# Kernel optimization log

Measured on AMD Instinct MI355X. Metric: run time of the kernel, lower is better.

Reference implementation:

```python
import jax, jax.numpy as jnp
import numpy as np

D_MODEL = 1024
NHEAD = 16
D_K = D_MODEL // NHEAD


def setup_inputs() -> dict:
    key = jax.random.key(0)
    ks = jax.random.split(key, 8)
    B, S = 2, 2048
    scale = 1.0 / np.sqrt(D_MODEL)
    return {
        "Q": jax.random.normal(ks[0], (B, S, D_MODEL), dtype=jnp.float32),
        "K": jax.random.normal(ks[1], (B, S, D_MODEL), dtype=jnp.float32),
        "V": jax.random.normal(ks[2], (B, S, D_MODEL), dtype=jnp.float32),
        "WQ": jax.random.normal(ks[3], (D_MODEL, D_MODEL), dtype=jnp.float32) * scale,
        "WK": jax.random.normal(ks[4], (D_MODEL, D_MODEL), dtype=jnp.float32) * scale,
        "WV": jax.random.normal(ks[5], (D_MODEL, D_MODEL), dtype=jnp.float32) * scale,
        "Wfc": jax.random.normal(ks[6], (D_MODEL, D_MODEL), dtype=jnp.float32) * scale,
        "bfc": jax.random.normal(ks[7], (D_MODEL,), dtype=jnp.float32) * 0.01,
    }


def reference(Q, K, V, WQ, WK, WV, Wfc, bfc):
    B, Sq, _ = Q.shape
    Skv = K.shape[1]
    # Linear projections (torch Linear: x @ W^T), split into heads: [B, H, S, d_k]
    q = (Q @ WQ.T).reshape(B, Sq, NHEAD, D_K).transpose(0, 2, 1, 3)
    k = (K @ WK.T).reshape(B, Skv, NHEAD, D_K).transpose(0, 2, 1, 3)
    v = (V @ WV.T).reshape(B, Skv, NHEAD, D_K).transpose(0, 2, 1, 3)
    # Scaled dot-product scores: [B, H, Sq, Skv]
    scores = jnp.einsum("bhqd,bhkd->bhqk", q, k) / jnp.sqrt(jnp.float32(D_K))
    # Causal mask (strict upper triangle -> -inf)
    causal = jnp.tril(jnp.ones((Sq, Skv), dtype=bool))
    scores = jnp.where(causal, scores, -jnp.inf)
    attn = jax.nn.softmax(scores, axis=-1)
    y = jnp.einsum("bhqk,bhkd->bhqd", attn, v)
    y = y.transpose(0, 2, 1, 3).reshape(B, Sq, D_MODEL)
    return y @ Wfc.T + bfc
```

## Files before the change

### kernel.cpp

```cpp
#include <hip/hip_runtime.h>

typedef __attribute__((ext_vector_type(8))) short bf16x8;
typedef __attribute__((ext_vector_type(4))) float f32x4;
typedef __attribute__((ext_vector_type(16))) float f32x16;

__device__ __forceinline__ ushort f2bf(float f) {
    union { float f; unsigned u; } x; x.f = f;
    unsigned r = x.u + 0x7fffu + ((x.u >> 16) & 1u);
    return (ushort)(r >> 16);
}

__device__ __forceinline__ void async16(const void* g, void* l) {
    __builtin_amdgcn_global_load_lds(
        (const __attribute__((address_space(1))) void*)g,
        (__attribute__((address_space(3))) void*)l, 16, 0, 0);
}

__device__ __forceinline__ f32x4 mfma16(bf16x8 a, bf16x8 b, f32x4 c) {
    return __builtin_amdgcn_mfma_f32_16x16x32_bf16(a, b, c, 0, 0, 0);
}
__device__ __forceinline__ f32x16 mfma32(bf16x8 a, bf16x8 b, f32x16 c) {
    return __builtin_amdgcn_mfma_f32_32x32x16_bf16(a, b, c, 0, 0, 0);
}

__device__ __forceinline__ f32x4 zero4() { f32x4 z = {0.f, 0.f, 0.f, 0.f}; return z; }

__global__ void cvt7_kernel(
    const float* __restrict__ s0, const float* __restrict__ s1, const float* __restrict__ s2,
    const float* __restrict__ s3, const float* __restrict__ s4, const float* __restrict__ s5,
    const float* __restrict__ s6,
    ushort* __restrict__ d0, ushort* __restrict__ d1, ushort* __restrict__ d2,
    ushort* __restrict__ d3, ushort* __restrict__ d4, ushort* __restrict__ d5,
    ushort* __restrict__ d6)
{
    int y = blockIdx.y;
    const float* s; ushort* d; int n4;
    if      (y == 0) { s = s0; d = d0; n4 = 1048576; }
    else if (y == 1) { s = s1; d = d1; n4 = 1048576; }
    else if (y == 2) { s = s2; d = d2; n4 = 1048576; }
    else if (y == 3) { s = s3; d = d3; n4 = 262144; }
    else if (y == 4) { s = s4; d = d4; n4 = 262144; }
    else if (y == 5) { s = s5; d = d5; n4 = 262144; }
    else             { s = s6; d = d6; n4 = 262144; }
    int i = blockIdx.x * 256 + threadIdx.x;
    if (i >= n4) return;
    float4 v = ((const float4*)s)[i];
    ushort4 o;
    o.x = f2bf(v.x); o.y = f2bf(v.y); o.z = f2bf(v.z); o.w = f2bf(v.w);
    ((ushort4*)d)[i] = o;
}

template<bool SWAP, int BK>
__device__ __forceinline__ void gemm_core(
    const ushort* __restrict__ A, const ushort* __restrict__ W,
    char* smem, int bm, int bn, int tid, f32x4 acc[4][4])
{
    constexpr int TILEB = 128 * BK * 2;
    constexpr int NSTEP = 1024 / BK;
    const int lane = tid & 63;
    const int wid  = tid >> 6;
    const int wr = wid >> 1, wc = wid & 1;
    const int l15 = lane & 15, g = lane >> 4;

    auto stage = [&](int kt, int b) {
        char* As = smem + b * (2 * TILEB);
        char* Bs = As + TILEB;
        if (BK == 64) {
            #pragma unroll
            for (int it = 0; it < 4; ++it) {
                int c = it * 256 + tid;
                int row = c >> 3, inner = c & 7;
                int srcoff = (inner ^ (row & 7)) * 16;
                async16((const char*)A + (size_t)(bm * 128 + row) * 2048 + kt * 128 + srcoff, As + c * 16);
                async16((const char*)W + (size_t)(bn * 128 + row) * 2048 + kt * 128 + srcoff, Bs + c * 16);
            }
        } else {
            #pragma unroll
            for (int it = 0; it < 2; ++it) {
                int c = it * 256 + tid;
                int row = c >> 2, inner = c & 3;
                int srcoff = (inner ^ (row & 3)) * 16;
                async16((const char*)A + (size_t)(bm * 128 + row) * 2048 + kt * 64 + srcoff, As + c * 16);
                async16((const char*)W + (size_t)(bn * 128 + row) * 2048 + kt * 64 + srcoff, Bs + c * 16);
            }
        }
    };

    stage(0, 0);
    __syncthreads();

    for (int kt = 0; kt < NSTEP; ++kt) {
        const int cur = kt & 1;
        if (kt < NSTEP - 1) stage(kt + 1, cur ^ 1);

        const char* As = smem + cur * (2 * TILEB);
        const char* Bs = As + TILEB;
        constexpr int KS = BK / 32;
        bf16x8 af[4][KS], bfr[4][KS];
        #pragma unroll
        for (int mt = 0; mt < 4; ++mt)
            #pragma unroll
            for (int ks = 0; ks < KS; ++ks) {
                int row = wr * 64 + mt * 16 + l15;
                int byte;
                if (BK == 64) byte = (row * 128 + ks * 64 + g * 16) ^ ((row & 7) << 4);
                else          byte = (row * 64 + g * 16) ^ ((row & 3) << 4);
                af[mt][ks] = *(const bf16x8*)(As + byte);
            }
        #pragma unroll
        for (int nt = 0; nt < 4; ++nt)
            #pragma unroll
            for (int ks = 0; ks < KS; ++ks) {
                int row = wc * 64 + nt * 16 + l15;
                int byte;
                if (BK == 64) byte = (row * 128 + ks * 64 + g * 16) ^ ((row & 7) << 4);
                else          byte = (row * 64 + g * 16) ^ ((row & 3) << 4);
                bfr[nt][ks] = *(const bf16x8*)(Bs + byte);
            }
        #pragma unroll
        for (int mt = 0; mt < 4; ++mt)
            #pragma unroll
            for (int nt = 0; nt < 4; ++nt)
                #pragma unroll
                for (int ks = 0; ks < KS; ++ks) {
                    if (SWAP) acc[mt][nt] = mfma16(bfr[nt][ks], af[mt][ks], acc[mt][nt]);
                    else      acc[mt][nt] = mfma16(af[mt][ks], bfr[nt][ks], acc[mt][nt]);
                }
        __syncthreads();
    }
}

__global__ __launch_bounds__(256) void gemm_qkv(
    const ushort* __restrict__ Qb, const ushort* __restrict__ Kb, const ushort* __restrict__ Vb,
    const ushort* __restrict__ WQ, const ushort* __restrict__ WK, const ushort* __restrict__ WV,
    ushort* __restrict__ qhb, ushort* __restrict__ khb, ushort* __restrict__ vhT)
{
    __shared__ __align__(16) char smem[32768];
    const int tid = threadIdx.x;
    const int z  = blockIdx.x % 3;
    const int bm = blockIdx.x / 3;
    const int bn = blockIdx.y;
    const int lane = tid & 63;
    const int wid  = tid >> 6;
    const int wr = wid >> 1, wc = wid & 1;
    const int l15 = lane & 15, g = lane >> 4;

    const ushort* A  = (z == 0) ? Qb : (z == 1) ? Kb : Vb;
    const ushort* Wm = (z == 0) ? WQ : (z == 1) ? WK : WV;

    f32x4 acc[4][4];
    #pragma unroll
    for (int i = 0; i < 4; ++i)
        #pragma unroll
        for (int j = 0; j < 4; ++j) acc[i][j] = zero4();

    if (z == 2) {
        gemm_core<true, 32>(A, Wm, smem, bm, bn, tid, acc);
        #pragma unroll
        for (int mt = 0; mt < 4; ++mt)
            #pragma unroll
            for (int nt = 0; nt < 4; ++nt)
                #pragma unroll
                for (int j = 0; j < 4; ++j) {
                    int n = bn * 128 + wc * 64 + nt * 16 + g * 4 + j;
                    int m = bm * 128 + wr * 64 + mt * 16 + l15;
                    int b = m >> 11, s = m & 2047, h = (n >> 6) & 15, d = n & 63;
                    vhT[(((size_t)(b * 16 + h)) * 64 + d) * 2048 + s] = f2bf(acc[mt][nt][j]);
                }
    } else {
        gemm_core<false, 32>(A, Wm, smem, bm, bn, tid, acc);
        const float scale = (z == 0) ? 0.125f : 1.0f;
        ushort* outb = (z == 0) ? qhb : khb;
        #pragma unroll
        for (int mt = 0; mt < 4; ++mt)
            #pragma unroll
            for (int nt = 0; nt < 4; ++nt)
                #pragma unroll
                for (int j = 0; j < 4; ++j) {
                    int m = bm * 128 + wr * 64 + mt * 16 + g * 4 + j;
                    int n = bn * 128 + wc * 64 + nt * 16 + l15;
                    int b = m >> 11, s = m & 2047, h = n >> 6, d = n & 63;
                    outb[(((size_t)(b * 16 + h)) * 2048 + s) * 64 + d] = f2bf(acc[mt][nt][j] * scale);
                }
    }
}

__global__ __launch_bounds__(256) void gemm_fc(
    const ushort* __restrict__ A, const ushort* __restrict__ W,
    float* __restrict__ outf, const float* __restrict__ bias)
{
    __shared__ __align__(16) char smem[65536];
    const int tid = threadIdx.x;
    const int lane = tid & 63;
    const int wid  = tid >> 6;
    const int wr = wid >> 1, wc = wid & 1;
    const int l15 = lane & 15, g = lane >> 4;

    f32x4 acc[4][4];
    #pragma unroll
    for (int i = 0; i < 4; ++i)
        #pragma unroll
        for (int j = 0; j < 4; ++j) acc[i][j] = zero4();

    gemm_core<false, 64>(A, W, smem, blockIdx.x, blockIdx.y, tid, acc);

    #pragma unroll
    for (int mt = 0; mt < 4; ++mt)
        #pragma unroll
        for (int nt = 0; nt < 4; ++nt)
            #pragma unroll
            for (int j = 0; j < 4; ++j) {
                int m = blockIdx.x * 128 + wr * 64 + mt * 16 + g * 4 + j;
                int n = blockIdx.y * 128 + wc * 64 + nt * 16 + l15;
                outf[(size_t)m * 1024 + n] = acc[mt][nt][j] + bias[n];
            }
}

__global__ __launch_bounds__(512, 4) void attn_kernel(
    const ushort* __restrict__ qh, const ushort* __restrict__ kh,
    const ushort* __restrict__ vhT, ushort* __restrict__ yb)
{
    __shared__ __align__(16) char smem[65536];
    const int tid = threadIdx.x;
    const int lane = tid & 63, wid = tid >> 6;
    const int l31 = lane & 31;
    const int hi  = lane >> 5;
    const int group = wid >> 2;
    const int wq    = wid & 3;
    const int subkv = group * 64;
    const int bh = blockIdx.y;
    const int qt = (bh < 16) ? (int)blockIdx.x : 15 - (int)blockIdx.x;
    const size_t base = (size_t)bh * 2048 * 64;
    const int qrw = qt * 128 + wq * 32;

    auto stageK = [&](int t, int b) {
        char* Ks = smem + b * 16384;
        #pragma unroll
        for (int it = 0; it < 2; ++it) {
            int c = it * 512 + tid;
            int row = c >> 3, inner = c & 7;
            async16((const char*)kh + (base + (size_t)(t * 128 + row) * 64) * 2 + ((inner ^ (row & 7)) * 16),
                    Ks + c * 16);
        }
    };
    auto stageV = [&](int t, int b) {
        char* Vs = smem + 32768 + b * 16384;
        #pragma unroll
        for (int it = 0; it < 2; ++it) {
            int c = it * 512 + tid;
            int row = c >> 4, inner = c & 15;
            async16((const char*)vhT + (base + (size_t)row * 2048 + (size_t)t * 128) * 2 + ((inner ^ (row & 15)) * 16),
                    Vs + c * 16);
        }
    };

    bf16x8 qf[4];
    #pragma unroll
    for (int ks = 0; ks < 4; ++ks)
        qf[ks] = *(const bf16x8*)((const char*)qh + (base + (size_t)(qrw + l31) * 64) * 2 + ks * 32 + hi * 16);

    f32x16 o[2];
    #pragma unroll
    for (int r = 0; r < 16; ++r) { o[0][r] = 0.f; o[1][r] = 0.f; }
    float m_run = -1e30f, l_run = 0.f;

    stageK(0, 0); stageV(0, 0);
    __syncthreads();

    for (int i = 0; i <= qt; ++i) {
        const int cur = i & 1;
        if (i < qt) { stageK(i + 1, cur ^ 1); stageV(i + 1, cur ^ 1); }

        const int kv0 = i * 128 + subkv;
        if (kv0 <= qrw + 31) {
            const char* Ks = smem + cur * 16384;
            const char* Vs = smem + 32768 + cur * 16384;

            f32x16 st[2];
            #pragma unroll
            for (int r = 0; r < 16; ++r) { st[0][r] = 0.f; st[1][r] = 0.f; }
            __builtin_amdgcn_s_setprio(1);
            #pragma unroll
            for (int tt = 0; tt < 2; ++tt)
                #pragma unroll
                for (int ks = 0; ks < 4; ++ks) {
                    int krow = subkv + tt * 32 + l31;
                    int byte = (krow * 128 + ks * 32 + hi * 16) ^ ((krow & 7) << 4);
                    bf16x8 kf = *(const bf16x8*)(Ks + byte);
                    st[tt] = mfma32(kf, qf[ks], st[tt]);
                }
            __builtin_amdgcn_s_setprio(0);

            if (kv0 + 63 > qrw) {
                #pragma unroll
                for (int tt = 0; tt < 2; ++tt)
                    #pragma unroll
                    for (int r = 0; r < 16; ++r) {
                        int kv = kv0 + tt * 32 + (r & 3) + 8 * (r >> 2) + 4 * hi;
                        if (kv > qrw + l31) st[tt][r] = -1e30f;
                    }
            }

            float mx = st[0][0];
            #pragma unroll
            for (int tt = 0; tt < 2; ++tt)
                #pragma unroll
                for (int r = 0; r < 16; ++r) mx = fmaxf(mx, st[tt][r]);
            mx = fmaxf(mx, __shfl_xor(mx, 32));

            if (!__all(mx - m_run <= 8.0f)) {
                float mn = fmaxf(m_run, mx);
                float corr = __expf(m_run - mn);
                l_run *= corr;
                m_run = mn;
                #pragma unroll
                for (int r = 0; r < 16; ++r) {
                    int qsrc = (r & 3) + 8 * (r >> 2) + 4 * hi;
                    float c2 = __shfl(corr, qsrc);
                    o[0][r] *= c2; o[1][r] *= c2;
                }
            }

            float sum = 0.f;
            #pragma unroll
            for (int tt = 0; tt < 2; ++tt)
                #pragma unroll
                for (int r = 0; r < 16; ++r) {
                    float p = __expf(st[tt][r] - m_run);
                    st[tt][r] = p;
                    sum += p;
                }
            sum += __shfl_xor(sum, 32);
            l_run += sum;

            unsigned Wd[2][8], Xw[2][8];
            #pragma unroll
            for (int tt = 0; tt < 2; ++tt)
                #pragma unroll
                for (int k = 0; k < 8; ++k) {
                    unsigned w;
                    asm("v_cvt_pk_bf16_f32 %0, %1, %2" : "=v"(w) : "v"(st[tt][2 * k]), "v"(st[tt][2 * k + 1]));
                    Wd[tt][k] = w;
                }
            #pragma unroll
            for (int tt = 0; tt < 2; ++tt)
                #pragma unroll
                for (int k = 0; k < 8; ++k)
                    Xw[tt][k] = __shfl_xor((int)Wd[tt][k], 32);

            #pragma unroll
            for (int ks = 0; ks < 4; ++ks) {
                const int t2 = ks >> 1, bse = (ks & 1) * 4;
                unsigned w0 = hi ? Xw[t2][bse + 2] : Wd[t2][bse + 0];
                unsigned w1 = hi ? Xw[t2][bse + 3] : Wd[t2][bse + 1];
                unsigned w2 = hi ? Wd[t2][bse + 2] : Xw[t2][bse + 0];
                unsigned w3 = hi ? Wd[t2][bse + 3] : Xw[t2][bse + 1];
                unsigned pw[4] = {w0, w1, w2, w3};
                bf16x8 pf = *(const bf16x8*)pw;
                __builtin_amdgcn_s_setprio(1);
                #pragma unroll
                for (int dt = 0; dt < 2; ++dt) {
                    int vrow = dt * 32 + l31;
                    int colB = subkv * 2 + ks * 32 + hi * 16;
                    int byte = vrow * 256 + (colB ^ ((vrow & 15) << 4));
                    bf16x8 vf = *(const bf16x8*)(Vs + byte);
                    o[dt] = mfma32(pf, vf, o[dt]);
                }
                __builtin_amdgcn_s_setprio(0);
            }
        }
        __syncthreads();
    }

    float* oml = (float*)smem;
    if (group == 1) {
        float* p = oml + (size_t)(wq * 64 + lane) * 36;
        #pragma unroll
        for (int r = 0; r < 16; ++r) { p[r] = o[0][r]; p[16 + r] = o[1][r]; }
        p[32] = m_run; p[33] = l_run;
    }
    __syncthreads();
    if (group == 0) {
        const float* p = oml + (size_t)(wq * 64 + lane) * 36;
        float m1 = p[32], l1 = p[33];
        float mn = fmaxf(m_run, m1);
        float a0 = __expf(m_run - mn);
        float a1 = __expf(m1 - mn);
        float lt = l_run * a0 + l1 * a1;
        float invl = 1.0f / lt;

        const int b = bh >> 4, h = bh & 15;
        #pragma unroll
        for (int r = 0; r < 16; ++r) {
            int qsrc = (r & 3) + 8 * (r >> 2) + 4 * hi;
            float f0 = __shfl(a0, qsrc);
            float f1 = __shfl(a1, qsrc);
            float iv = __shfl(invl, qsrc);
            float v0 = (o[0][r] * f0 + p[r] * f1) * iv;
            float v1 = (o[1][r] * f0 + p[16 + r] * f1) * iv;
            int q = qrw + qsrc;
            size_t rowoff = ((size_t)(b * 2048 + q)) * 1024 + h * 64;
            yb[rowoff + l31]      = f2bf(v0);
            yb[rowoff + 32 + l31] = f2bf(v1);
        }
    }
}

extern "C" void kernel_launch(void* const* d_in, const int* in_sizes, int n_in,
                              void* d_out, int out_size, void* d_ws, size_t ws_size,
                              hipStream_t stream)
{
    const size_t MD = 4096ull * 1024;
    const size_t WD = 1024ull * 1024;
    ushort* ws  = (ushort*)d_ws;
    ushort* Qb  = ws;
    ushort* Kb  = Qb + MD;
    ushort* Vb  = Kb + MD;
    ushort* qhb = Vb + MD;
    ushort* khb = qhb + MD;
    ushort* vhT = khb + MD;
    ushort* WQb = vhT + MD;
    ushort* WKb = WQb + WD;
    ushort* WVb = WKb + WD;
    ushort* Wfb = WVb + WD;
    ushort* yb  = Qb;

    cvt7_kernel<<<dim3(4096, 7), 256, 0, stream>>>(
        (const float*)d_in[0], (const float*)d_in[1], (const float*)d_in[2],
        (const float*)d_in[3], (const float*)d_in[4], (const float*)d_in[5],
        (const float*)d_in[6],
        Qb, Kb, Vb, WQb, WKb, WVb, Wfb);

    gemm_qkv<<<dim3(96, 8), 256, 0, stream>>>(Qb, Kb, Vb, WQb, WKb, WVb, qhb, khb, vhT);
    attn_kernel<<<dim3(16, 32), 512, 0, stream>>>(qhb, khb, vhT, yb);
    gemm_fc<<<dim3(32, 8), 256, 0, stream>>>(yb, Wfb, (float*)d_out, (const float*)d_in[7]);
}
```

Baseline: 121.8 us.

## Triple-buffer GEMM and attention loads with vmcnt waits and pair causal tiles

Both GEMMs now share a three-stage cp.async-style pipeline at BK=32. A raw s_waitcnt vmcnt barrier lets the next tile's loads stay in flight while the current tile is consumed. The attention kernel also gets a three-stage K/V ring, and each block now processes a pair of causal query tiles (qt and 15-qt) in sequence, halving the grid to balance work per block. LDS use in attention grows to about 132KB, which limits occupancy, and launch bounds are changed.

```diff
diff --git a/kernel.cpp b/kernel.cpp
--- a/kernel.cpp
+++ b/kernel.cpp
@@ -24,6 +24,16 @@
 }
 
 __device__ __forceinline__ f32x4 zero4() { f32x4 z = {0.f, 0.f, 0.f, 0.f}; return z; }
+
+#define PIPE_BARRIER(cond_more)                                          \
+    do {                                                                 \
+        if (cond_more) asm volatile("s_waitcnt vmcnt(4)" ::: "memory");  \
+        else           asm volatile("s_waitcnt vmcnt(0)" ::: "memory");  \
+        asm volatile("s_waitcnt lgkmcnt(0)" ::: "memory");               \
+        __builtin_amdgcn_sched_barrier(0);                               \
+        __builtin_amdgcn_s_barrier();                                    \
+        __builtin_amdgcn_sched_barrier(0);                               \
+    } while (0)
 
 __global__ void cvt7_kernel(
     const float* __restrict__ s0, const float* __restrict__ s1, const float* __restrict__ s2,
@@ -50,92 +60,67 @@
     ((ushort4*)d)[i] = o;
 }
 
-template<bool SWAP, int BK>
+template<bool SWAP>
 __device__ __forceinline__ void gemm_core(
     const ushort* __restrict__ A, const ushort* __restrict__ W,
     char* smem, int bm, int bn, int tid, f32x4 acc[4][4])
 {
-    constexpr int TILEB = 128 * BK * 2;
-    constexpr int NSTEP = 1024 / BK;
     const int lane = tid & 63;
     const int wid  = tid >> 6;
     const int wr = wid >> 1, wc = wid & 1;
     const int l15 = lane & 15, g = lane >> 4;
 
-    auto stage = [&](int kt, int b) {
-        char* As = smem + b * (2 * TILEB);
-        char* Bs = As + TILEB;
-        if (BK == 64) {
-            #pragma unroll
-            for (int it = 0; it < 4; ++it) {
-                int c = it * 256 + tid;
-                int row = c >> 3, inner = c & 7;
-                int srcoff = (inner ^ (row & 7)) * 16;
-                async16((const char*)A + (size_t)(bm * 128 + row) * 2048 + kt * 128 + srcoff, As + c * 16);
-                async16((const char*)W + (size_t)(bn * 128 + row) * 2048 + kt * 128 + srcoff, Bs + c * 16);
+    auto stage = [&](int kt) {
+        char* As = smem + (kt % 3) * 16384;
+        char* Bs = As + 8192;
+        #pragma unroll
+        for (int it = 0; it < 2; ++it) {
+            int c = it * 256 + tid;
+            int row = c >> 2, inner = c & 3;
+            int srcoff = (inner ^ (row & 3)) * 16;
+            async16((const char*)A + (size_t)(bm * 128 + row) * 2048 + kt * 64 + srcoff, As + c * 16);
+            async16((const char*)W + (size_t)(bn * 128 + row) * 2048 + kt * 64 + srcoff, Bs + c * 16);
+        }
+    };
+
+    stage(0);
+    stage(1);
+
+    for (int kt = 0; kt < 32; ++kt) {
+        PIPE_BARRIER(kt < 31);
+        if (kt < 30) stage(kt + 2);
+
+        const char* As = smem + (kt % 3) * 16384;
+        const char* Bs = As + 8192;
+        bf16x8 af[4], bfr[4];
+        #pragma unroll
+        for (int mt = 0; mt < 4; ++mt) {
+            int row = wr * 64 + mt * 16 + l15;
+            af[mt] = *(const bf16x8*)(As + ((row * 64 + g * 16) ^ ((row & 3) << 4)));
+        }
+        #pragma unroll
+        for (int nt = 0; nt < 4; ++nt) {
+            int row = wc * 64 + nt * 16 + l15;
+            bfr[nt] = *(const bf16x8*)(Bs + ((row * 64 + g * 16) ^ ((row & 3) << 4)));
+        }
+        __builtin_amdgcn_s_setprio(1);
+        #pragma unroll
+        for (int mt = 0; mt < 4; ++mt)
+            #pragma unroll
+            for (int nt = 0; nt < 4; ++nt) {
+                if (SWAP) acc[mt][nt] = mfma16(bfr[nt], af[mt], acc[mt][nt]);
+                else      acc[mt][nt] = mfma16(af[mt], bfr[nt], acc[mt][nt]);
             }
-        } else {
-            #pragma unroll
-            for (int it = 0; it < 2; ++it) {
-                int c = it * 256 + tid;
-                int row = c >> 2, inner = c & 3;
-                int srcoff = (inner ^ (row & 3)) * 16;
-                async16((const char*)A + (size_t)(bm * 128 + row) * 2048 + kt * 64 + srcoff, As + c * 16);
-                async16((const char*)W + (size_t)(bn * 128 + row) * 2048 + kt * 64 + srcoff, Bs + c * 16);
-            }
-        }
-    };
-
-    stage(0, 0);
-    __syncthreads();
-
-    for (int kt = 0; kt < NSTEP; ++kt) {
-        const int cur = kt & 1;
-        if (kt < NSTEP - 1) stage(kt + 1, cur ^ 1);
-
-        const char* As = smem + cur * (2 * TILEB);
-        const char* Bs = As + TILEB;
-        constexpr int KS = BK / 32;
-        bf16x8 af[4][KS], bfr[4][KS];
-        #pragma unroll
-        for (int mt = 0; mt < 4; ++mt)
-            #pragma unroll
-            for (int ks = 0; ks < KS; ++ks) {
-                int row = wr * 64 + mt * 16 + l15;
-                int byte;
-                if (BK == 64) byte = (row * 128 + ks * 64 + g * 16) ^ ((row & 7) << 4);
-                else          byte = (row * 64 + g * 16) ^ ((row & 3) << 4);
-                af[mt][ks] = *(const bf16x8*)(As + byte);
-            }
-        #pragma unroll
-        for (int nt = 0; nt < 4; ++nt)
-            #pragma unroll
-            for (int ks = 0; ks < KS; ++ks) {
-                int row = wc * 64 + nt * 16 + l15;
-                int byte;
-                if (BK == 64) byte = (row * 128 + ks * 64 + g * 16) ^ ((row & 7) << 4);
-                else          byte = (row * 64 + g * 16) ^ ((row & 3) << 4);
-                bfr[nt][ks] = *(const bf16x8*)(Bs + byte);
-            }
-        #pragma unroll
-        for (int mt = 0; mt < 4; ++mt)
-            #pragma unroll
-            for (int nt = 0; nt < 4; ++nt)
-                #pragma unroll
-                for (int ks = 0; ks < KS; ++ks) {
-                    if (SWAP) acc[mt][nt] = mfma16(bfr[nt][ks], af[mt][ks], acc[mt][nt]);
-                    else      acc[mt][nt] = mfma16(af[mt][ks], bfr[nt][ks], acc[mt][nt]);
-                }
-        __syncthreads();
+        __builtin_amdgcn_s_setprio(0);
     }
 }
 
-__global__ __launch_bounds__(256) void gemm_qkv(
+__global__ __launch_bounds__(256, 2) void gemm_qkv(
     const ushort* __restrict__ Qb, const ushort* __restrict__ Kb, const ushort* __restrict__ Vb,
     const ushort* __restrict__ WQ, const ushort* __restrict__ WK, const ushort* __restrict__ WV,
     ushort* __restrict__ qhb, ushort* __restrict__ khb, ushort* __restrict__ vhT)
 {
-    __shared__ __align__(16) char smem[32768];
+    __shared__ __align__(16) char smem[49152];
     const int tid = threadIdx.x;
     const int z  = blockIdx.x % 3;
     const int bm = blockIdx.x / 3;
@@ -155,7 +140,7 @@
         for (int j = 0; j < 4; ++j) acc[i][j] = zero4();
 
     if (z == 2) {
-        gemm_core<true, 32>(A, Wm, smem, bm, bn, tid, acc);
+        gemm_core<true>(A, Wm, smem, bm, bn, tid, acc);
         #pragma unroll
         for (int mt = 0; mt < 4; ++mt)
             #pragma unroll
@@ -168,7 +153,7 @@
                     vhT[(((size_t)(b * 16 + h)) * 64 + d) * 2048 + s] = f2bf(acc[mt][nt][j]);
                 }
     } else {
-        gemm_core<false, 32>(A, Wm, smem, bm, bn, tid, acc);
+        gemm_core<false>(A, Wm, smem, bm, bn, tid, acc);
         const float scale = (z == 0) ? 0.125f : 1.0f;
         ushort* outb = (z == 0) ? qhb : khb;
         #pragma unroll
@@ -185,11 +170,11 @@
     }
 }
 
-__global__ __launch_bounds__(256) void gemm_fc(
+__global__ __launch_bounds__(256, 2) void gemm_fc(
     const ushort* __restrict__ A, const ushort* __restrict__ W,
     float* __restrict__ outf, const float* __restrict__ bias)
 {
-    __shared__ __align__(16) char smem[65536];
+    __shared__ __align__(16) char smem[49152];
     const int tid = threadIdx.x;
     const int lane = tid & 63;
     const int wid  = tid >> 6;
@@ -202,7 +187,7 @@
         #pragma unroll
         for (int j = 0; j < 4; ++j) acc[i][j] = zero4();
 
-    gemm_core<false, 64>(A, W, smem, blockIdx.x, blockIdx.y, tid, acc);
+    gemm_core<false>(A, W, smem, blockIdx.x, blockIdx.y, tid, acc);
 
     #pragma unroll
     for (int mt = 0; mt < 4; ++mt)
@@ -216,11 +201,11 @@
             }
 }
 
-__global__ __launch_bounds__(512, 4) void attn_kernel(
+__global__ __launch_bounds__(512, 2) void attn_kernel(
     const ushort* __restrict__ qh, const ushort* __restrict__ kh,
     const ushort* __restrict__ vhT, ushort* __restrict__ yb)
 {
-    __shared__ __align__(16) char smem[65536];
+    __shared__ __align__(16) char smem[135168];
     const int tid = threadIdx.x;
     const int lane = tid & 63, wid = tid >> 6;
     const int l31 = lane & 31;
@@ -229,12 +214,12 @@
     const int wq    = wid & 3;
     const int subkv = group * 64;
     const int bh = blockIdx.y;
-    const int qt = (bh < 16) ? (int)blockIdx.x : 15 - (int)blockIdx.x;
     const size_t base = (size_t)bh * 2048 * 64;
-    const int qrw = qt * 128 + wq * 32;
-
-    auto stageK = [&](int t, int b) {
-        char* Ks = smem + b * 16384;
+    const int b_ = bh >> 4, h_ = bh & 15;
+    float* oml = (float*)(smem + 98304);
+
+    auto stageK = [&](int t) {
+        char* Ks = smem + (t % 3) * 32768;
         #pragma unroll
         for (int it = 0; it < 2; ++it) {
             int c = it * 512 + tid;
@@ -243,8 +228,8 @@
                     Ks + c * 16);
         }
     };
-    auto stageV = [&](int t, int b) {
-        char* Vs = smem + 32768 + b * 16384;
+    auto stageV = [&](int t) {
+        char* Vs = smem + (t % 3) * 32768 + 16384;
         #pragma unroll
         for (int it = 0; it < 2; ++it) {
             int c = it * 512 + tid;
@@ -254,155 +239,158 @@
         }
     };
 
-    bf16x8 qf[4];
-    #pragma unroll
-    for (int ks = 0; ks < 4; ++ks)
-        qf[ks] = *(const bf16x8*)((const char*)qh + (base + (size_t)(qrw + l31) * 64) * 2 + ks * 32 + hi * 16);
-
-    f32x16 o[2];
-    #pragma unroll
-    for (int r = 0; r < 16; ++r) { o[0][r] = 0.f; o[1][r] = 0.f; }
-    float m_run = -1e30f, l_run = 0.f;
-
-    stageK(0, 0); stageV(0, 0);
-    __syncthreads();
-
-    for (int i = 0; i <= qt; ++i) {
-        const int cur = i & 1;
-        if (i < qt) { stageK(i + 1, cur ^ 1); stageV(i + 1, cur ^ 1); }
-
-        const int kv0 = i * 128 + subkv;
-        if (kv0 <= qrw + 31) {
-            const char* Ks = smem + cur * 16384;
-            const char* Vs = smem + 32768 + cur * 16384;
-
-            f32x16 st[2];
-            #pragma unroll
-            for (int r = 0; r < 16; ++r) { st[0][r] = 0.f; st[1][r] = 0.f; }
-            __builtin_amdgcn_s_setprio(1);
-            #pragma unroll
-            for (int tt = 0; tt < 2; ++tt)
+    for (int p = 0; p < 2; ++p) {
+        const int qt  = (p == 0) ? (int)blockIdx.x : 15 - (int)blockIdx.x;
+        const int qrw = qt * 128 + wq * 32;
+
+        bf16x8 qf[4];
+        #pragma unroll
+        for (int ks = 0; ks < 4; ++ks)
+            qf[ks] = *(const bf16x8*)((const char*)qh + (base + (size_t)(qrw + l31) * 64) * 2 + ks * 32 + hi * 16);
+
+        f32x16 o[2];
+        #pragma unroll
+        for (int r = 0; r < 16; ++r) { o[0][r] = 0.f; o[1][r] = 0.f; }
+        float m_run = -1e30f, l_run = 0.f;
+
+        stageK(0); stageV(0);
+        if (qt >= 1) { stageK(1); stageV(1); }
+
+        for (int t = 0; t <= qt; ++t) {
+            PIPE_BARRIER(t < qt);
+            if (t + 2 <= qt) { stageK(t + 2); stageV(t + 2); }
+
+            const int kv0 = t * 128 + subkv;
+            if (kv0 <= qrw + 31) {
+                const char* Ks = smem + (t % 3) * 32768;
+                const char* Vs = Ks + 16384;
+
+                f32x16 st[2];
+                #pragma unroll
+                for (int r = 0; r < 16; ++r) { st[0][r] = 0.f; st[1][r] = 0.f; }
+                __builtin_amdgcn_s_setprio(1);
+                #pragma unroll
+                for (int tt = 0; tt < 2; ++tt)
+                    #pragma unroll
+                    for (int ks = 0; ks < 4; ++ks) {
+                        int krow = subkv + tt * 32 + l31;
+                        int byte = (krow * 128 + ks * 32 + hi * 16) ^ ((krow & 7) << 4);
+                        bf16x8 kf = *(const bf16x8*)(Ks + byte);
+                        st[tt] = mfma32(kf, qf[ks], st[tt]);
+                    }
+                __builtin_amdgcn_s_setprio(0);
+
+                if (kv0 + 63 > qrw) {
+                    #pragma unroll
+                    for (int tt = 0; tt < 2; ++tt)
+                        #pragma unroll
+                        for (int r = 0; r < 16; ++r) {
+                            int kv = kv0 + tt * 32 + (r & 3) + 8 * (r >> 2) + 4 * hi;
+                            if (kv > qrw + l31) st[tt][r] = -1e30f;
+                        }
+                }
+
+                float mx = st[0][0];
+                #pragma unroll
+                for (int tt = 0; tt < 2; ++tt)
+                    #pragma unroll
+                    for (int r = 0; r < 16; ++r) mx = fmaxf(mx, st[tt][r]);
+                mx = fmaxf(mx, __shfl_xor(mx, 32));
+
+                if (!__all(mx - m_run <= 8.0f)) {
+                    float mn = fmaxf(m_run, mx);
+                    float corr = __expf(m_run - mn);
+                    l_run *= corr;
+                    m_run = mn;
+                    #pragma unroll
+                    for (int r = 0; r < 16; ++r) {
+                        int qsrc = (r & 3) + 8 * (r >> 2) + 4 * hi;
+                        float c2 = __shfl(corr, qsrc);
+                        o[0][r] *= c2; o[1][r] *= c2;
+                    }
+                }
+
+                float sum = 0.f;
+                #pragma unroll
+                for (int tt = 0; tt < 2; ++tt)
+                    #pragma unroll
+                    for (int r = 0; r < 16; ++r) {
+                        float pw = __expf(st[tt][r] - m_run);
+                        st[tt][r] = pw;
+                        sum += pw;
+                    }
+                sum += __shfl_xor(sum, 32);
+                l_run += sum;
+
+                unsigned Wd[2][8], Xw[2][8];
+                #pragma unroll
+                for (int tt = 0; tt < 2; ++tt)
+                    #pragma unroll
+                    for (int k = 0; k < 8; ++k) {
+                        unsigned w;
+                        asm("v_cvt_pk_bf16_f32 %0, %1, %2" : "=v"(w) : "v"(st[tt][2 * k]), "v"(st[tt][2 * k + 1]));
+                        Wd[tt][k] = w;
+                    }
+                #pragma unroll
+                for (int tt = 0; tt < 2; ++tt)
+                    #pragma unroll
+                    for (int k = 0; k < 8; ++k)
+                        Xw[tt][k] = __shfl_xor((int)Wd[tt][k], 32);
+
                 #pragma unroll
                 for (int ks = 0; ks < 4; ++ks) {
-                    int krow = subkv + tt * 32 + l31;
-                    int byte = (krow * 128 + ks * 32 + hi * 16) ^ ((krow & 7) << 4);
-                    bf16x8 kf = *(const bf16x8*)(Ks + byte);
-                    st[tt] = mfma32(kf, qf[ks], st[tt]);
-                }
-            __builtin_amdgcn_s_setprio(0);
-
-            if (kv0 + 63 > qrw) {
-                #pragma unroll
-                for (int tt = 0; tt < 2; ++tt)
-                    #pragma unroll
-                    for (int r = 0; r < 16; ++r) {
-                        int kv = kv0 + tt * 32 + (r & 3) + 8 * (r >> 2) + 4 * hi;
-                        if (kv > qrw + l31) st[tt][r] = -1e30f;
+                    const int t2 = ks >> 1, bse = (ks & 1) * 4;
+                    unsigned w0 = hi ? Xw[t2][bse + 2] : Wd[t2][bse + 0];
+                    unsigned w1 = hi ? Xw[t2][bse + 3] : Wd[t2][bse + 1];
+                    unsigned w2 = hi ? Wd[t2][bse + 2] : Xw[t2][bse + 0];
+                    unsigned w3 = hi ? Wd[t2][bse + 3] : Xw[t2][bse + 1];
+                    unsigned pw4[4] = {w0, w1, w2, w3};
+                    bf16x8 pf = *(const bf16x8*)pw4;
+                    __builtin_amdgcn_s_setprio(1);
+                    #pragma unroll
+                    for (int dt = 0; dt < 2; ++dt) {
+                        int vrow = dt * 32 + l31;
+                        int colB = subkv * 2 + ks * 32 + hi * 16;
+                        int byte = vrow * 256 + (colB ^ ((vrow & 15) << 4));
+                        bf16x8 vf = *(const bf16x8*)(Vs + byte);
+                        o[dt] = mfma32(pf, vf, o[dt]);
                     }
-            }
-
-            float mx = st[0][0];
-            #pragma unroll
-            for (int tt = 0; tt < 2; ++tt)
-                #pragma unroll
-                for (int r = 0; r < 16; ++r) mx = fmaxf(mx, st[tt][r]);
-            mx = fmaxf(mx, __shfl_xor(mx, 32));
-
-            if (!__all(mx - m_run <= 8.0f)) {
-                float mn = fmaxf(m_run, mx);
-                float corr = __expf(m_run - mn);
-                l_run *= corr;
-                m_run = mn;
-                #pragma unroll
-                for (int r = 0; r < 16; ++r) {
-                    int qsrc = (r & 3) + 8 * (r >> 2) + 4 * hi;
-                    float c2 = __shfl(corr, qsrc);
-                    o[0][r] *= c2; o[1][r] *= c2;
+                    __builtin_amdgcn_s_setprio(0);
                 }
             }
-
-            float sum = 0.f;
-            #pragma unroll
-            for (int tt = 0; tt < 2; ++tt)
-                #pragma unroll
-                for (int r = 0; r < 16; ++r) {
-                    float p = __expf(st[tt][r] - m_run);
-                    st[tt][r] = p;
-                    sum += p;
-                }
-            sum += __shfl_xor(sum, 32);
-            l_run += sum;
-
-            unsigned Wd[2][8], Xw[2][8];
-            #pragma unroll
-            for (int tt = 0; tt < 2; ++tt)
-                #pragma unroll
-                for (int k = 0; k < 8; ++k) {
-                    unsigned w;
-                    asm("v_cvt_pk_bf16_f32 %0, %1, %2" : "=v"(w) : "v"(st[tt][2 * k]), "v"(st[tt][2 * k + 1]));
-                    Wd[tt][k] = w;
-                }
-            #pragma unroll
-            for (int tt = 0; tt < 2; ++tt)
-                #pragma unroll
-                for (int k = 0; k < 8; ++k)
-                    Xw[tt][k] = __shfl_xor((int)Wd[tt][k], 32);
-
-            #pragma unroll
-            for (int ks = 0; ks < 4; ++ks) {
-                const int t2 = ks >> 1, bse = (ks & 1) * 4;
-                unsigned w0 = hi ? Xw[t2][bse + 2] : Wd[t2][bse + 0];
-                unsigned w1 = hi ? Xw[t2][bse + 3] : Wd[t2][bse + 1];
-                unsigned w2 = hi ? Wd[t2][bse + 2] : Xw[t2][bse + 0];
-                unsigned w3 = hi ? Wd[t2][bse + 3] : Xw[t2][bse + 1];
-                unsigned pw[4] = {w0, w1, w2, w3};
-                bf16x8 pf = *(const bf16x8*)pw;
-                __builtin_amdgcn_s_setprio(1);
-                #pragma unroll
-                for (int dt = 0; dt < 2; ++dt) {
-                    int vrow = dt * 32 + l31;
-                    int colB = subkv * 2 + ks * 32 + hi * 16;
-                    int byte = vrow * 256 + (colB ^ ((vrow & 15) << 4));
-                    bf16x8 vf = *(const bf16x8*)(Vs + byte);
-                    o[dt] = mfma32(pf, vf, o[dt]);
-                }
-                __builtin_amdgcn_s_setprio(0);
+        }
+
+        __syncthreads();
+        if (group == 1) {
+            float* pp = oml + (size_t)(wq * 64 + lane) * 36;
+            #pragma unroll
+            for (int r = 0; r < 16; ++r) { pp[r] = o[0][r]; pp[16 + r] = o[1][r]; }
+            pp[32] = m_run; pp[33] = l_run;
+        }
+        __syncthreads();
+        if (group == 0) {
+            const float* pp = oml + (size_t)(wq * 64 + lane) * 36;
+            float m1 = pp[32], l1 = pp[33];
+            float mn = fmaxf(m_run, m1);
+            float a0 = __expf(m_run - mn);
+            float a1 = __expf(m1 - mn);
+            float lt = l_run * a0 + l1 * a1;
+            float invl = 1.0f / lt;
+            #pragma unroll
+            for (int r = 0; r < 16; ++r) {
+                int qsrc = (r & 3) + 8 * (r >> 2) + 4 * hi;
+                float f0 = __shfl(a0, qsrc);
+                float f1 = __shfl(a1, qsrc);
+                float iv = __shfl(invl, qsrc);
+                float v0 = (o[0][r] * f0 + pp[r] * f1) * iv;
+                float v1 = (o[1][r] * f0 + pp[16 + r] * f1) * iv;
+                int q = qrw + qsrc;
+                size_t rowoff = ((size_t)(b_ * 2048 + q)) * 1024 + h_ * 64;
+                yb[rowoff + l31]      = f2bf(v0);
+                yb[rowoff + 32 + l31] = f2bf(v1);
             }
         }
         __syncthreads();
-    }
-
-    float* oml = (float*)smem;
-    if (group == 1) {
-        float* p = oml + (size_t)(wq * 64 + lane) * 36;
-        #pragma unroll
-        for (int r = 0; r < 16; ++r) { p[r] = o[0][r]; p[16 + r] = o[1][r]; }
-        p[32] = m_run; p[33] = l_run;
-    }
-    __syncthreads();
-    if (group == 0) {
-        const float* p = oml + (size_t)(wq * 64 + lane) * 36;
-        float m1 = p[32], l1 = p[33];
-        float mn = fmaxf(m_run, m1);
-        float a0 = __expf(m_run - mn);
-        float a1 = __expf(m1 - mn);
-        float lt = l_run * a0 + l1 * a1;
-        float invl = 1.0f / lt;
-
-        const int b = bh >> 4, h = bh & 15;
-        #pragma unroll
-        for (int r = 0; r < 16; ++r) {
-            int qsrc = (r & 3) + 8 * (r >> 2) + 4 * hi;
-            float f0 = __shfl(a0, qsrc);
-            float f1 = __shfl(a1, qsrc);
-            float iv = __shfl(invl, qsrc);
-            float v0 = (o[0][r] * f0 + p[r] * f1) * iv;
-            float v1 = (o[1][r] * f0 + p[16 + r] * f1) * iv;
-            int q = qrw + qsrc;
-            size_t rowoff = ((size_t)(b * 2048 + q)) * 1024 + h * 64;
-            yb[rowoff + l31]      = f2bf(v0);
-            yb[rowoff + 32 + l31] = f2bf(v1);
-        }
     }
 }
 
@@ -432,6 +420,6 @@
         Qb, Kb, Vb, WQb, WKb, WVb, Wfb);
 
     gemm_qkv<<<dim3(96, 8), 256, 0, stream>>>(Qb, Kb, Vb, WQb, WKb, WVb, qhb, khb, vhT);
-    attn_kernel<<<dim3(16, 32), 512, 0, stream>>>(qhb, khb, vhT, yb);
+    attn_kernel<<<dim3(8, 32), 512, 0, stream>>>(qhb, khb, vhT, yb);
     gemm_fc<<<dim3(32, 8), 256, 0, stream>>>(yb, Wfb, (float*)d_out, (const float*)d_in[7]);
 }
```

Measured after the change: 117.0 us. 1.04x faster.
